# Kernel optimization log

Measured on AMD Instinct MI355X. Metric: run time of the kernel, lower is better.

The kernel has to match this reference:

```python
import jax, jax.numpy as jnp
import numpy as np

B, C, T = 16, 768, 9
S = T * T * T            # 729 tokens
H = 8                    # heads
E = 3                    # experts
HID = C * 4              # expert hidden dim (mult=4)


def setup_inputs() -> dict:
    key = jax.random.key(0)
    ks = jax.random.split(key, 8)
    w = lambda k, sh: (jax.random.normal(k, sh, jnp.float32) * 0.02)
    return {
        "x": jax.random.normal(ks[0], (B, C, T, T, T), jnp.float32),
        "ln_gamma": jnp.ones((C, T, T, T), jnp.float32),
        "ln_beta": jnp.zeros((C, T, T, T), jnp.float32),
        "w_qkv": w(ks[1], (C, 3 * C)),
        "w_out": w(ks[2], (C, C)),
        "w_gate": w(ks[3], (C, E)),
        "b_gate": jnp.zeros((E,), jnp.float32),
        "w1": w(ks[4], (E, C, HID)),
        "b1": jnp.zeros((E, HID), jnp.float32),
        "w2": w(ks[5], (E, HID, C)),
        "b2": jnp.zeros((E, C), jnp.float32),
    }


def reference(x, ln_gamma, ln_beta, w_qkv, w_out, w_gate, b_gate, w1, b1, w2, b2):
    b = x.shape[0]
    # LayerNorm over (C, T, H, W) per batch element, affine params [C,T,T,T]
    mu = jnp.mean(x, axis=(1, 2, 3, 4), keepdims=True)
    var = jnp.var(x, axis=(1, 2, 3, 4), keepdims=True)
    xn = (x - mu) * jax.lax.rsqrt(var + 1e-5) * ln_gamma + ln_beta

    # ---- attention (NOTE: source applies no 1/sqrt(d) scaling) ----
    tok = xn.reshape(b, C, S).transpose(0, 2, 1)                 # [b,s,c]
    qkv = (tok @ w_qkv).reshape(b, S, 3, H, C // H)              # [b,s,3,h,d]
    q = qkv[:, :, 0].transpose(0, 2, 1, 3)                       # [b,h,s,d]
    k = qkv[:, :, 1].transpose(0, 2, 1, 3)
    v = qkv[:, :, 2].transpose(0, 2, 1, 3)
    attn = jax.nn.softmax(jnp.einsum('bhqd,bhkd->bhqk', q, k), axis=-1)
    ctx = jnp.einsum('bhqk,bhkd->bqhd', attn, v).reshape(b, S, C)
    attn_out = (ctx @ w_out).transpose(0, 2, 1).reshape(b, C, T, T, T)
    x2 = x + attn_out                                            # residual (dropout = eval identity)

    # ---- switch-MoE (top-1 gate, all experts computed densely then masked) ----
    tok2 = x2.reshape(b, C, S).transpose(0, 2, 1)                # [b,s,c]
    gate = jax.nn.softmax(tok2 @ w_gate + b_gate, axis=-1)       # [b,s,E]
    mask = jax.nn.one_hot(jnp.argmax(gate, axis=-1), E, dtype=gate.dtype)
    mg = gate * mask
    denom = jnp.sum(mg, axis=0, keepdims=True) + 1e-6            # sum over dim 0, per source
    gate_scores = mg / denom * b                                 # capacity = int(1.0 * b)

    hmid = jax.nn.gelu(jnp.einsum('bsc,ech->bseh', tok2, w1) + b1, approximate=False)
    eout = jnp.einsum('bseh,ehc->bsec', hmid, w2) + b2           # [b,s,E,c]
    moe = jnp.einsum('bse,bsec->bsc', gate_scores, eout)         # weighted mix over experts

    out = x2 + moe.transpose(0, 2, 1).reshape(b, C, T, T, T)
    return out
```

## Files before the change

### kernel.cpp

```cpp
#include <hip/hip_runtime.h>

typedef __bf16 bf16;
typedef __bf16 bf16x4_t __attribute__((ext_vector_type(4)));
typedef __bf16 bf16x8_t __attribute__((ext_vector_type(8)));
typedef float f32x4 __attribute__((ext_vector_type(4)));

#define DEVI __device__ __forceinline__

#define N_B   16
#define N_C   768
#define N_S   729
#define N_TOK 11664
#define TOKP  11776
#define N_H   8
#define N_D   96
#define N_HID 3072
#define MOE_TILES 94
#define GATE_BLOCKS 183

#define OFF_WQKVH 0ull
#define OFF_WQKVL 3538944ull
#define OFF_WOUTH 7077888ull
#define OFF_WOUTL 8257536ull
#define OFF_W1T   9437184ull
#define OFF_W2T   23592960ull
#define OFF_XTOK  37748736ull
#define OFF_R3    73924608ull
#define OFF_TOKH  OFF_R3
#define OFF_TOKL  (OFF_R3 + 18087936ull)
#define OFF_VTH   OFF_R3
#define OFF_VTL   (OFF_R3 + 18087936ull)
#define OFF_T2H   OFF_R3
#define OFF_QKH   110100480ull
#define OFF_QKL   146276352ull
#define OFF_VPH   182452224ull
#define OFF_VPL   200540160ull
#define OFF_CTXH  OFF_VPH
#define OFF_CTXL  OFF_VPL
#define OFF_HMID  OFF_QKH
#define OFF_X2    218628096ull
#define OFF_STATS 254803968ull
#define OFF_DENOM (OFF_STATS + 256ull)
#define OFF_SEL   (OFF_STATS + 16384ull)
#define OFF_PVAL  (OFF_SEL + 65536ull)
#define OFF_GSV   (OFF_PVAL + 65536ull)
#define OFF_PERM  (OFF_GSV + 65536ull)
#define OFF_CNT   (OFF_PERM + 65536ull)

DEVI f32x4 mfma16(bf16x8_t a, bf16x8_t b, f32x4 c) {
  return __builtin_amdgcn_mfma_f32_16x16x32_bf16(a, b, c, 0, 0, 0);
}
DEVI bf16 f2bf(float f) { return (bf16)f; }
DEVI float bf2f(bf16 h) { return (float)h; }
#define GLDS(gp, lp) __builtin_amdgcn_global_load_lds( \
    (__attribute__((address_space(1))) void*)(gp),     \
    (__attribute__((address_space(3))) void*)(lp), 16, 0, 0)

template<bool SPLIT>
__global__ void kxpose(const float* __restrict__ in, bf16* __restrict__ oh,
                       bf16* __restrict__ ol, int R, int Cc) {
  __shared__ float T[32][33];
  int c0 = blockIdx.x * 32, r0 = blockIdx.y * 32;
  int tx = threadIdx.x, ty = threadIdx.y;
#pragma unroll
  for (int i = 0; i < 4; i++)
    T[ty + i * 8][tx] = in[(size_t)(r0 + ty + i * 8) * Cc + c0 + tx];
  __syncthreads();
#pragma unroll
  for (int i = 0; i < 4; i++) {
    float v = T[tx][ty + i * 8];
    size_t o = (size_t)(c0 + ty + i * 8) * R + r0 + tx;
    bf16 hh = f2bf(v);
    oh[o] = hh;
    if constexpr (SPLIT) ol[o] = f2bf(v - bf2f(hh));
  }
}

__global__ __launch_bounds__(256) void ln_stats(const float* __restrict__ x,
                                                double* __restrict__ stats) {
  int b = blockIdx.x >> 7, ch = blockIdx.x & 127;
  const float* xb = x + (size_t)b * 559872;
  int start = ch * 4374;
  float s = 0.f, ss = 0.f;
  for (int i = start + threadIdx.x; i < start + 4374; i += 256) {
    float v = xb[i];
    s += v; ss += v * v;
  }
#pragma unroll
  for (int o = 32; o > 0; o >>= 1) { s += __shfl_down(s, o); ss += __shfl_down(ss, o); }
  __shared__ float rs[4], rss[4];
  int w = threadIdx.x >> 6;
  if ((threadIdx.x & 63) == 0) { rs[w] = s; rss[w] = ss; }
  __syncthreads();
  if (threadIdx.x == 0) {
    atomicAdd(&stats[b * 2 + 0], (double)(rs[0] + rs[1] + rs[2] + rs[3]));
    atomicAdd(&stats[b * 2 + 1], (double)(rss[0] + rss[1] + rss[2] + rss[3]));
  }
}

__global__ void ln_apply(const float* __restrict__ x, const float* __restrict__ g,
                         const float* __restrict__ be, const double* __restrict__ stats,
                         float* __restrict__ xtok, bf16* __restrict__ th, bf16* __restrict__ tl) {
  __shared__ float TN[32][33], TX[32][33];
  int b = blockIdx.z, c0 = blockIdx.y * 32, s0 = blockIdx.x * 32;
  double mu = stats[b * 2] * (1.0 / 559872.0);
  double var = stats[b * 2 + 1] * (1.0 / 559872.0) - mu * mu;
  float rstd = (float)(1.0 / sqrt(var + 1e-5));
  float muf = (float)mu;
  int tx = threadIdx.x, ty = threadIdx.y;
  size_t bo = (size_t)b * 559872;
#pragma unroll
  for (int i = 0; i < 4; i++) {
    int c = c0 + ty + i * 8, s = s0 + tx;
    float v = 0.f, xn = 0.f;
    if (s < N_S) {
      v = x[bo + (size_t)c * 729 + s];
      xn = (v - muf) * rstd * g[(size_t)c * 729 + s] + be[(size_t)c * 729 + s];
    }
    TX[ty + i * 8][tx] = v;
    TN[ty + i * 8][tx] = xn;
  }
  __syncthreads();
#pragma unroll
  for (int i = 0; i < 4; i++) {
    int s = s0 + ty + i * 8;
    if (s < N_S) {
      size_t tok = (size_t)b * 729 + s;
      int c = c0 + tx;
      float xv = TX[tx][ty + i * 8];
      float xn = TN[tx][ty + i * 8];
      xtok[tok * 768 + c] = xv;
      bf16 hh = f2bf(xn);
      th[tok * 768 + c] = hh;
      tl[tok * 768 + c] = f2bf(xn - bf2f(hh));
    }
  }
}

enum { EPI_HL = 0, EPI_ATTNOUT = 1 };

template<int EPI, bool SPLIT>
__global__ __launch_bounds__(256, 2)
void gemm_k(const bf16* __restrict__ Ah, const bf16* __restrict__ Al,
            const bf16* __restrict__ Bh, const bf16* __restrict__ Bl,
            int M, int N, int K,
            bf16* __restrict__ o0, bf16* __restrict__ o1, float* __restrict__ of,
            const float* __restrict__ fa) {
  __shared__ bf16 Ash[4096], Bsh[4096], Asl[4096], Bsl[4096];
  const int t = threadIdx.x;
  const int lane = t & 63, w = t >> 6;
  const int wr = (w >> 1) << 6, wc = (w & 1) << 6;
  const int lr = lane & 15, lg = lane >> 4;
  const size_t arow = (size_t)blockIdx.y * 128;
  const size_t brow = (size_t)blockIdx.x * 128;
  const int sr = t >> 2, sc4 = (t & 3) << 3;
  const bf16* pA0 = Ah + (arow + sr) * (size_t)K + sc4;
  const bf16* pA1 = pA0 + ((size_t)K << 6);
  const bf16* pB0 = Bh + (brow + sr) * (size_t)K + sc4;
  const bf16* pB1 = pB0 + ((size_t)K << 6);
  const bf16 *pA0l = nullptr, *pA1l = nullptr, *pB0l = nullptr, *pB1l = nullptr;
  if constexpr (SPLIT) {
    pA0l = Al + (arow + sr) * (size_t)K + sc4; pA1l = pA0l + ((size_t)K << 6);
    pB0l = Bl + (brow + sr) * (size_t)K + sc4; pB1l = pB0l + ((size_t)K << 6);
  }
  f32x4 acc[4][4] = {};
  for (int k0 = 0; k0 < K; k0 += 32) {
    __syncthreads();
    GLDS(pA0 + k0, &Ash[t * 8]);
    GLDS(pA1 + k0, &Ash[2048 + t * 8]);
    GLDS(pB0 + k0, &Bsh[t * 8]);
    GLDS(pB1 + k0, &Bsh[2048 + t * 8]);
    if constexpr (SPLIT) {
      GLDS(pA0l + k0, &Asl[t * 8]);
      GLDS(pA1l + k0, &Asl[2048 + t * 8]);
      GLDS(pB0l + k0, &Bsl[t * 8]);
      GLDS(pB1l + k0, &Bsl[2048 + t * 8]);
    }
    asm volatile("s_waitcnt vmcnt(0)" ::: "memory");
    __syncthreads();
    bf16x8_t af[4], bq[4], afl[4], bql[4];
#pragma unroll
    for (int m = 0; m < 4; m++) {
      int row = wr + m * 16 + lr;
      af[m] = *(const bf16x8_t*)&Ash[row * 32 + lg * 8];
      if constexpr (SPLIT) afl[m] = *(const bf16x8_t*)&Asl[row * 32 + lg * 8];
    }
#pragma unroll
    for (int n = 0; n < 4; n++) {
      int row = wc + n * 16 + lr;
      bq[n] = *(const bf16x8_t*)&Bsh[row * 32 + lg * 8];
      if constexpr (SPLIT) bql[n] = *(const bf16x8_t*)&Bsl[row * 32 + lg * 8];
    }
#pragma unroll
    for (int m = 0; m < 4; m++)
#pragma unroll
      for (int n = 0; n < 4; n++) {
        acc[m][n] = mfma16(af[m], bq[n], acc[m][n]);
        if constexpr (SPLIT) {
          acc[m][n] = mfma16(af[m], bql[n], acc[m][n]);
          acc[m][n] = mfma16(afl[m], bq[n], acc[m][n]);
        }
      }
  }
#pragma unroll
  for (int m = 0; m < 4; m++) {
#pragma unroll
    for (int r = 0; r < 4; r++) {
      int gr = (int)arow + wr + m * 16 + lg * 4 + r;
      if (gr >= M) continue;
#pragma unroll
      for (int n = 0; n < 4; n++) {
        int gc = (int)brow + wc + n * 16 + lr;
        float v = acc[m][n][r];
        size_t oidx = (size_t)gr * N + gc;
        if constexpr (EPI == EPI_HL) {
          bf16 hh = f2bf(v);
          o0[oidx] = hh;
          o1[oidx] = f2bf(v - bf2f(hh));
        } else {
          float x2v = v + fa[(size_t)gr * 768 + gc];
          of[(size_t)gr * 768 + gc] = x2v;
          o0[(size_t)gr * 768 + gc] = f2bf(x2v);
        }
      }
    }
  }
}

__global__ __launch_bounds__(256, 2)
void gemm_moe1(const bf16* __restrict__ Ah, const bf16* __restrict__ W1T,
               const float* __restrict__ b1, const int* __restrict__ perm,
               const int* __restrict__ poff, bf16* __restrict__ hmid) {
  const int arow = blockIdx.y * 128;
  if (arow >= poff[3]) return;
  const int e = (arow >= poff[1]) + (arow >= poff[2]);
  const bf16* Bh = W1T + (size_t)e * 3072 * 768;
  const float* bias = b1 + e * 3072;
  __shared__ bf16 Ash[4096], Bsh[4096];
  const int t = threadIdx.x;
  const int lane = t & 63, w = t >> 6;
  const int wr = (w >> 1) << 6, wc = (w & 1) << 6;
  const int lr = lane & 15, lg = lane >> 4;
  const size_t brow = (size_t)blockIdx.x * 128;
  const int sr = t >> 2, sc4 = (t & 3) << 3;
  int i0 = perm[arow + sr];       if (i0 < 0) i0 = 0;
  int i1 = perm[arow + sr + 64];  if (i1 < 0) i1 = 0;
  const bf16* pA0 = Ah + (size_t)i0 * 768 + sc4;
  const bf16* pA1 = Ah + (size_t)i1 * 768 + sc4;
  const bf16* pB0 = Bh + (brow + sr) * 768 + sc4;
  const bf16* pB1 = pB0 + (768ull << 6);
  f32x4 acc[4][4] = {};
  for (int k0 = 0; k0 < 768; k0 += 32) {
    __syncthreads();
    GLDS(pA0 + k0, &Ash[t * 8]);
    GLDS(pA1 + k0, &Ash[2048 + t * 8]);
    GLDS(pB0 + k0, &Bsh[t * 8]);
    GLDS(pB1 + k0, &Bsh[2048 + t * 8]);
    asm volatile("s_waitcnt vmcnt(0)" ::: "memory");
    __syncthreads();
    bf16x8_t af[4], bq[4];
#pragma unroll
    for (int m = 0; m < 4; m++)
      af[m] = *(const bf16x8_t*)&Ash[(wr + m * 16 + lr) * 32 + lg * 8];
#pragma unroll
    for (int n = 0; n < 4; n++)
      bq[n] = *(const bf16x8_t*)&Bsh[(wc + n * 16 + lr) * 32 + lg * 8];
#pragma unroll
    for (int m = 0; m < 4; m++)
#pragma unroll
      for (int n = 0; n < 4; n++)
        acc[m][n] = mfma16(af[m], bq[n], acc[m][n]);
  }
#pragma unroll
  for (int m = 0; m < 4; m++)
#pragma unroll
    for (int r = 0; r < 4; r++) {
      int gr = arow + wr + m * 16 + lg * 4 + r;
#pragma unroll
      for (int n = 0; n < 4; n++) {
        int gc = (int)brow + wc + n * 16 + lr;
        float z = acc[m][n][r] + bias[gc];
        float gl = 0.5f * z * (1.f + erff(z * 0.7071067811865476f));
        hmid[(size_t)gr * 3072 + gc] = f2bf(gl);
      }
    }
}

__global__ __launch_bounds__(256, 2)
void gemm_moe2(const bf16* __restrict__ hmid, const bf16* __restrict__ W2T,
               const float* __restrict__ b2, const int* __restrict__ perm,
               const int* __restrict__ poff, const float* __restrict__ gsv,
               float* __restrict__ moe) {
  const int arow = blockIdx.y * 128;
  if (arow >= poff[3]) return;
  const int e = (arow >= poff[1]) + (arow >= poff[2]);
  const bf16* Bh = W2T + (size_t)e * 768 * 3072;
  const float* bias = b2 + e * 768;
  __shared__ bf16 Ash[4096], Bsh[4096];
  const int t = threadIdx.x;
  const int lane = t & 63, w = t >> 6;
  const int wr = (w >> 1) << 6, wc = (w & 1) << 6;
  const int lr = lane & 15, lg = lane >> 4;
  const size_t brow = (size_t)blockIdx.x * 128;
  const int sr = t >> 2, sc4 = (t & 3) << 3;
  const bf16* pA0 = hmid + (size_t)(arow + sr) * 3072 + sc4;
  const bf16* pA1 = pA0 + (3072ull << 6);
  const bf16* pB0 = Bh + (brow + sr) * 3072 + sc4;
  const bf16* pB1 = pB0 + (3072ull << 6);
  f32x4 acc[4][4] = {};
  for (int k0 = 0; k0 < 3072; k0 += 32) {
    __syncthreads();
    GLDS(pA0 + k0, &Ash[t * 8]);
    GLDS(pA1 + k0, &Ash[2048 + t * 8]);
    GLDS(pB0 + k0, &Bsh[t * 8]);
    GLDS(pB1 + k0, &Bsh[2048 + t * 8]);
    asm volatile("s_waitcnt vmcnt(0)" ::: "memory");
    __syncthreads();
    bf16x8_t af[4], bq[4];
#pragma unroll
    for (int m = 0; m < 4; m++)
      af[m] = *(const bf16x8_t*)&Ash[(wr + m * 16 + lr) * 32 + lg * 8];
#pragma unroll
    for (int n = 0; n < 4; n++)
      bq[n] = *(const bf16x8_t*)&Bsh[(wc + n * 16 + lr) * 32 + lg * 8];
#pragma unroll
    for (int m = 0; m < 4; m++)
#pragma unroll
      for (int n = 0; n < 4; n++)
        acc[m][n] = mfma16(af[m], bq[n], acc[m][n]);
  }
#pragma unroll
  for (int m = 0; m < 4; m++)
#pragma unroll
    for (int r = 0; r < 4; r++) {
      int gr = arow + wr + m * 16 + lg * 4 + r;
      int tok = perm[gr];
      if (tok < 0) continue;
      float gv = gsv[tok];
#pragma unroll
      for (int n = 0; n < 4; n++) {
        int gc = (int)brow + wc + n * 16 + lr;
        moe[(size_t)tok * 768 + gc] = (acc[m][n][r] + bias[gc]) * gv;
      }
    }
}

__global__ __launch_bounds__(256) void repack_v(const bf16* __restrict__ vph,
    const bf16* __restrict__ vpl, bf16* __restrict__ vth, bf16* __restrict__ vtl) {
  __shared__ bf16 Lh[96][40], Ll[96][40];
  int t = threadIdx.x;
  int bh = blockIdx.y, b = bh >> 3, h = bh & 7;
  int s0 = blockIdx.x * 32;
  for (int v = t; v < 384; v += 256) {
    int e0 = v * 8;
    int r = e0 / 96;
    int c = e0 - r * 96;
    size_t src = ((size_t)b * 729 + s0 + r) * 768 + h * 96 + c;
    bf16x8_t xh = *(const bf16x8_t*)&vph[src];
    bf16x8_t xl = *(const bf16x8_t*)&vpl[src];
    bool ok = (s0 + r) < N_S;
#pragma unroll
    for (int j = 0; j < 8; j++) {
      Lh[c + j][r] = ok ? xh[j] : f2bf(0.f);
      Ll[c + j][r] = ok ? xl[j] : f2bf(0.f);
    }
  }
  __syncthreads();
  for (int vv = t; vv < 768; vv += 256) {
    int e0 = vv * 4;
    int d = e0 >> 5, sl = e0 & 31;
    bf16x4_t ohv, olv;
#pragma unroll
    for (int j = 0; j < 4; j++) { ohv[j] = Lh[d][sl + j]; olv[j] = Ll[d][sl + j]; }
    size_t dst = (size_t)bh * (96ull * 736ull) + (size_t)d * 736 + s0 + sl;
    *(bf16x4_t*)&vth[dst] = ohv;
    *(bf16x4_t*)&vtl[dst] = olv;
  }
}

DEVI int pslot(int w, int s) { return ((s >> 9) << 11) + (w << 9) + (s & 511); }

__global__ __launch_bounds__(256, 3)
void attn(const bf16* __restrict__ qkh, const bf16* __restrict__ qkl,
          const bf16* __restrict__ vth, const bf16* __restrict__ vtl,
          bf16* __restrict__ ch, bf16* __restrict__ cl) {
  __shared__ bf16 Ksh[6144], Ksl[6144], Vsh[6144], Vsl[6144];
  const int t = threadIdx.x, lane = t & 63, w = t >> 6;
  const int lr = lane & 15, lg = lane >> 4;
  const int bh = blockIdx.y, b = bh >> 3, h = bh & 7;
  const int q0 = blockIdx.x * 64;
  const size_t tokbase = (size_t)b * 729;
  const int qr = w * 16 + lr;
  const size_t qrow = (tokbase + q0 + qr) * 1536ull + (size_t)h * 96;
  bf16x8_t qh[3], ql[3];
#pragma unroll
  for (int ks = 0; ks < 3; ks++) {
    qh[ks] = *(const bf16x8_t*)&qkh[qrow + ks * 32 + lg * 8];
    ql[ks] = *(const bf16x8_t*)&qkl[qrow + ks * 32 + lg * 8];
  }

  auto loadK = [&](int kt) {
    const int kv0 = kt * 64;
#pragma unroll
    for (int chk = 0; chk < 3; chk++) {
      int kv = t >> 2, dg = t & 3;
      int sdg = dg ^ (kv & 3);
      size_t ksrc = (tokbase + kv0 + kv) * 1536ull + 768ull + (size_t)h * 96 + chk * 32 + (sdg << 3);
      int ldsoff = chk * 2048 + t * 8;
      GLDS(qkh + ksrc, &Ksh[ldsoff]);
      GLDS(qkl + ksrc, &Ksl[ldsoff]);
    }
  };
  auto loadV = [&](int kt) {
    const int kv0 = kt * 64;
#pragma unroll
    for (int chk = 0; chk < 3; chk++) {
      int ldsoff = chk * 2048 + t * 8;
      int d = ldsoff >> 6;
      int grp = (ldsoff >> 3) & 7;
      int sg = grp ^ (d & 7);
      size_t vsrc = (size_t)bh * (96ull * 736ull) + (size_t)d * 736 + kv0 + (sg << 3);
      GLDS(vth + vsrc, &Vsh[ldsoff]);
      GLDS(vtl + vsrc, &Vsl[ldsoff]);
    }
  };

  float mrow[4] = {-1e30f, -1e30f, -1e30f, -1e30f};
  float lpart[4] = {0.f, 0.f, 0.f, 0.f};
  f32x4 octx[6] = {};

  loadK(0);
  asm volatile("s_waitcnt vmcnt(0)" ::: "memory");
  __syncthreads();
  loadV(0);

  for (int kt = 0; kt < 12; kt++) {
    const int kv0 = kt * 64;
    f32x4 sc[4];
    __builtin_amdgcn_s_setprio(1);
#pragma unroll
    for (int cf = 0; cf < 4; cf++) {
      f32x4 a = {0.f, 0.f, 0.f, 0.f};
      int kvrow = cf * 16 + lr;
#pragma unroll
      for (int ks = 0; ks < 3; ks++) {
        int slot = ks * 2048 + kvrow * 32 + ((lg ^ (kvrow & 3)) << 3);
        bf16x8_t kh = *(const bf16x8_t*)&Ksh[slot];
        bf16x8_t kl = *(const bf16x8_t*)&Ksl[slot];
        a = mfma16(qh[ks], kh, a);
        a = mfma16(qh[ks], kl, a);
        a = mfma16(ql[ks], kh, a);
      }
      if (kv0 + kvrow >= N_S) { a[0] = -1e30f; a[1] = -1e30f; a[2] = -1e30f; a[3] = -1e30f; }
      sc[cf] = a;
    }
    __builtin_amdgcn_s_setprio(0);
    float lmax[4];
#pragma unroll
    for (int r = 0; r < 4; r++)
      lmax[r] = fmaxf(fmaxf(sc[0][r], sc[1][r]), fmaxf(sc[2][r], sc[3][r]));
    bool ok = (lmax[0] <= mrow[0] + 8.f) && (lmax[1] <= mrow[1] + 8.f) &&
              (lmax[2] <= mrow[2] + 8.f) && (lmax[3] <= mrow[3] + 8.f);
    if (!__all(ok)) {
      float escv[4];
#pragma unroll
      for (int r = 0; r < 4; r++) {
        float a = lmax[r];
#pragma unroll
        for (int o = 1; o < 16; o <<= 1) a = fmaxf(a, __shfl_xor(a, o));
        float mn = fmaxf(mrow[r], a);
        escv[r] = __expf(mrow[r] - mn);
        mrow[r] = mn;
        lpart[r] *= escv[r];
      }
#pragma unroll
      for (int df = 0; df < 6; df++)
#pragma unroll
        for (int r = 0; r < 4; r++) octx[df][r] *= escv[r];
    }
#pragma unroll
    for (int cf = 0; cf < 4; cf++)
#pragma unroll
      for (int r = 0; r < 4; r++) {
        float p = __expf(sc[cf][r] - mrow[r]);
        sc[cf][r] = p;
        lpart[r] += p;
      }
    asm volatile("s_waitcnt vmcnt(0)" ::: "memory");
    __syncthreads();
#pragma unroll
    for (int cf = 0; cf < 4; cf++)
#pragma unroll
      for (int r = 0; r < 4; r++) {
        int qloc = lg * 4 + r;
        int kvg = (cf << 1) | (lr >> 3);
        int xw = (qloc ^ (qloc >> 2)) & 7;
        int slot = qloc * 64 + (((kvg ^ xw) << 3) | (lr & 7));
        float p = sc[cf][r];
        bf16 hp = f2bf(p);
        int ps = pslot(w, slot);
        Ksh[ps] = hp;
        Ksl[ps] = f2bf(p - bf2f(hp));
      }
    asm volatile("s_waitcnt lgkmcnt(0)" ::: "memory");
    __builtin_amdgcn_sched_barrier(0);
    bf16x8_t pah[2], pal[2];
#pragma unroll
    for (int ks = 0; ks < 2; ks++) {
      int xr = (lr ^ (lr >> 2)) & 7;
      int slot = lr * 64 + ((((ks << 2) | lg) ^ xr) << 3);
      int ps = pslot(w, slot);
      pah[ks] = *(const bf16x8_t*)&Ksh[ps];
      pal[ks] = *(const bf16x8_t*)&Ksl[ps];
    }
    asm volatile("s_waitcnt lgkmcnt(0)" ::: "memory");
    __builtin_amdgcn_sched_barrier(0);
    if (kt < 11) loadK(kt + 1);
    __builtin_amdgcn_s_setprio(1);
#pragma unroll
    for (int df = 0; df < 6; df++) {
      int dd = df * 16 + lr;
#pragma unroll
      for (int ks = 0; ks < 2; ks++) {
        int slot = dd * 64 + ((((ks << 2) | lg) ^ (dd & 7)) << 3);
        bf16x8_t vh = *(const bf16x8_t*)&Vsh[slot];
        bf16x8_t vl = *(const bf16x8_t*)&Vsl[slot];
        octx[df] = mfma16(pah[ks], vh, octx[df]);
        octx[df] = mfma16(pah[ks], vl, octx[df]);
        octx[df] = mfma16(pal[ks], vh, octx[df]);
      }
    }
    __builtin_amdgcn_s_setprio(0);
    if (kt < 11) {
      asm volatile("s_waitcnt vmcnt(0)" ::: "memory");
      __syncthreads();
      loadV(kt + 1);
    }
  }
  float lrow[4];
#pragma unroll
  for (int r = 0; r < 4; r++) {
    float a = lpart[r];
#pragma unroll
    for (int o = 1; o < 16; o <<= 1) a += __shfl_xor(a, o);
    lrow[r] = a;
  }
#pragma unroll
  for (int r = 0; r < 4; r++) {
    int qloc = w * 16 + lg * 4 + r;
    if (q0 + qloc >= N_S) continue;
    size_t orow = (tokbase + q0 + qloc) * 768ull + (size_t)h * 96;
    float inv = 1.f / lrow[r];
#pragma unroll
    for (int df = 0; df < 6; df++) {
      float v = octx[df][r] * inv;
      bf16 hh = f2bf(v);
      ch[orow + df * 16 + lr] = hh;
      cl[orow + df * 16 + lr] = f2bf(v - bf2f(hh));
    }
  }
}

__global__ __launch_bounds__(256) void gate_k(const float* __restrict__ x2,
    const float* __restrict__ wg, const float* __restrict__ bg,
    int* __restrict__ sel, float* __restrict__ pval, float* __restrict__ denom,
    int* __restrict__ cnt) {
  int lane = threadIdx.x & 63, w = threadIdx.x >> 6;
  float wv[12][3];
#pragma unroll
  for (int j = 0; j < 12; j++) {
    int c = lane + j * 64;
    const float* wgc = wg + c * 3;
    wv[j][0] = wgc[0]; wv[j][1] = wgc[1]; wv[j][2] = wgc[2];
  }
  float bg0 = bg[0], bg1 = bg[1], bg2 = bg[2];
  int cloc0 = 0, cloc1 = 0, cloc2 = 0;
  int base_tok = (blockIdx.x * 4 + w) * 16;
  for (int it = 0; it < 16; it++) {
    int tok = base_tok + it;
    if (tok >= N_TOK) break;
    const float* row = x2 + (size_t)tok * 768;
    double a0 = 0, a1 = 0, a2 = 0;
#pragma unroll
    for (int j = 0; j < 12; j++) {
      float xv = row[lane + j * 64];
      a0 += (double)(xv * wv[j][0]);
      a1 += (double)(xv * wv[j][1]);
      a2 += (double)(xv * wv[j][2]);
    }
#pragma unroll
    for (int o = 32; o > 0; o >>= 1) {
      a0 += __shfl_down(a0, o);
      a1 += __shfl_down(a1, o);
      a2 += __shfl_down(a2, o);
    }
    if (lane == 0) {
      float g0 = (float)a0 + bg0, g1 = (float)a1 + bg1, g2 = (float)a2 + bg2;
      float mx = fmaxf(g0, fmaxf(g1, g2));
      float e0 = __expf(g0 - mx), e1 = __expf(g1 - mx), e2 = __expf(g2 - mx);
      float inv = 1.f / (e0 + e1 + e2);
      int am = 0; float pm = e0;
      if (e1 > pm) { pm = e1; am = 1; }
      if (e2 > pm) { pm = e2; am = 2; }
      float p = pm * inv;
      sel[tok] = am;
      pval[tok] = p;
      int s = tok - (tok / 729) * 729;
      atomicAdd(&denom[s * 3 + am], p);
      cloc0 += (am == 0); cloc1 += (am == 1); cloc2 += (am == 2);
    }
  }
  __shared__ int bc[3];
  if (threadIdx.x == 0) { bc[0] = 0; bc[1] = 0; bc[2] = 0; }
  __syncthreads();
  if (lane == 0) {
    if (cloc0) atomicAdd(&bc[0], cloc0);
    if (cloc1) atomicAdd(&bc[1], cloc1);
    if (cloc2) atomicAdd(&bc[2], cloc2);
  }
  __syncthreads();
  if (threadIdx.x < 3 && bc[threadIdx.x]) atomicAdd(&cnt[threadIdx.x], bc[threadIdx.x]);
}

__global__ void moe_scan(const int* __restrict__ cnt, int* __restrict__ poff) {
  int p1 = (cnt[0] + 127) & ~127;
  int p2 = p1 + ((cnt[1] + 127) & ~127);
  int p3 = p2 + ((cnt[2] + 127) & ~127);
  poff[0] = 0; poff[1] = p1; poff[2] = p2; poff[3] = p3;
}

__global__ __launch_bounds__(256) void moe_scatter(const int* __restrict__ sel,
                            const float* __restrict__ pval,
                            const float* __restrict__ denom, const int* __restrict__ poff,
                            int* __restrict__ cur, int* __restrict__ perm,
                            float* __restrict__ gsv) {
  int tok = blockIdx.x * 256 + threadIdx.x;
  int lane = threadIdx.x & 63, w = threadIdx.x >> 6;
  bool valid = tok < N_TOK;
  int e = valid ? sel[tok] : -1;
  if (valid) {
    int s = tok - (tok / 729) * 729;
    gsv[tok] = pval[tok] * 16.f / (denom[s * 3 + e] + 1e-6f);
  }
  unsigned long long m0 = __ballot(e == 0);
  unsigned long long m1 = __ballot(e == 1);
  unsigned long long m2 = __ballot(e == 2);
  __shared__ int wcnt[4][3], wbase[4][3];
  if (lane == 0) {
    wcnt[w][0] = __popcll(m0);
    wcnt[w][1] = __popcll(m1);
    wcnt[w][2] = __popcll(m2);
  }
  __syncthreads();
  if (threadIdx.x < 3) {
    int x = threadIdx.x;
    int c0 = wcnt[0][x], c1 = wcnt[1][x], c2 = wcnt[2][x], c3 = wcnt[3][x];
    int base = atomicAdd(&cur[x], c0 + c1 + c2 + c3);
    wbase[0][x] = base;
    wbase[1][x] = base + c0;
    wbase[2][x] = base + c0 + c1;
    wbase[3][x] = base + c0 + c1 + c2;
  }
  __syncthreads();
  if (valid) {
    unsigned long long lt = (lane == 0) ? 0ull : ((~0ull) >> (64 - lane));
    unsigned long long me = (e == 0) ? m0 : (e == 1) ? m1 : m2;
    int pos = wbase[w][e] + __popcll(me & lt);
    perm[poff[e] + pos] = tok;
  }
}

__global__ void final_k(const float* __restrict__ x2, const float* __restrict__ moe,
                        float* __restrict__ out) {
  __shared__ float L[32][33];
  int b = blockIdx.z, c0 = blockIdx.y * 32, s0 = blockIdx.x * 32;
  int tx = threadIdx.x, ty = threadIdx.y;
#pragma unroll
  for (int i = 0; i < 4; i++) {
    int s = s0 + ty + i * 8;
    float v = 0.f;
    if (s < N_S) {
      size_t tok = (size_t)b * 729 + s;
      v = x2[tok * 768 + c0 + tx] + moe[tok * 768 + c0 + tx];
    }
    L[ty + i * 8][tx] = v;
  }
  __syncthreads();
#pragma unroll
  for (int i = 0; i < 4; i++) {
    int s = s0 + tx;
    int c = c0 + ty + i * 8;
    if (s < N_S) out[((size_t)b * 768 + c) * 729 + s] = L[tx][ty + i * 8];
  }
}

extern "C" void kernel_launch(void* const* d_in, const int* in_sizes, int n_in,
                              void* d_out, int out_size, void* d_ws, size_t ws_size,
                              hipStream_t stream) {
  (void)in_sizes; (void)n_in; (void)out_size; (void)ws_size;
  const float* x     = (const float*)d_in[0];
  const float* lng   = (const float*)d_in[1];
  const float* lnb   = (const float*)d_in[2];
  const float* wqkv  = (const float*)d_in[3];
  const float* wout  = (const float*)d_in[4];
  const float* wgate = (const float*)d_in[5];
  const float* bgate = (const float*)d_in[6];
  const float* w1    = (const float*)d_in[7];
  const float* b1    = (const float*)d_in[8];
  const float* w2    = (const float*)d_in[9];
  const float* b2    = (const float*)d_in[10];
  float* out = (float*)d_out;
  char* ws = (char*)d_ws;

  bf16* WQKVH = (bf16*)(ws + OFF_WQKVH);
  bf16* WQKVL = (bf16*)(ws + OFF_WQKVL);
  bf16* WOUTH = (bf16*)(ws + OFF_WOUTH);
  bf16* WOUTL = (bf16*)(ws + OFF_WOUTL);
  bf16* W1T   = (bf16*)(ws + OFF_W1T);
  bf16* W2T   = (bf16*)(ws + OFF_W2T);
  float* XTOK = (float*)(ws + OFF_XTOK);
  float* MOE  = (float*)(ws + OFF_XTOK);
  bf16* TOKH  = (bf16*)(ws + OFF_TOKH);
  bf16* TOKL  = (bf16*)(ws + OFF_TOKL);
  bf16* VTH   = (bf16*)(ws + OFF_VTH);
  bf16* VTL   = (bf16*)(ws + OFF_VTL);
  bf16* T2H   = (bf16*)(ws + OFF_T2H);
  bf16* QKH   = (bf16*)(ws + OFF_QKH);
  bf16* QKL   = (bf16*)(ws + OFF_QKL);
  bf16* VPH   = (bf16*)(ws + OFF_VPH);
  bf16* VPL   = (bf16*)(ws + OFF_VPL);
  bf16* CTXH  = (bf16*)(ws + OFF_CTXH);
  bf16* CTXL  = (bf16*)(ws + OFF_CTXL);
  bf16* HMID  = (bf16*)(ws + OFF_HMID);
  float* X2   = (float*)(ws + OFF_X2);
  double* STATS = (double*)(ws + OFF_STATS);
  float* DENOM  = (float*)(ws + OFF_DENOM);
  int*   SEL    = (int*)(ws + OFF_SEL);
  float* PVAL   = (float*)(ws + OFF_PVAL);
  float* GSV    = (float*)(ws + OFF_GSV);
  int*   PERM   = (int*)(ws + OFF_PERM);
  int*   CNT    = (int*)(ws + OFF_CNT);
  int*   POFF   = CNT + 4;
  int*   CUR    = CNT + 8;

  hipMemsetAsync(ws + OFF_STATS, 0, 16384, stream);
  hipMemsetAsync(ws + OFF_CNT, 0, 64, stream);
  hipMemsetAsync(ws + OFF_PERM, 0xFF, MOE_TILES * 128 * 4, stream);

  dim3 tb(32, 8);
  kxpose<true><<<dim3(72, 24), tb, 0, stream>>>(wqkv, WQKVH, WQKVL, 768, 2304);
  kxpose<true><<<dim3(24, 24), tb, 0, stream>>>(wout, WOUTH, WOUTL, 768, 768);
  for (int e = 0; e < 3; e++) {
    kxpose<false><<<dim3(96, 24), tb, 0, stream>>>(w1 + (size_t)e * 768 * 3072,
        W1T + (size_t)e * 3072 * 768, nullptr, 768, 3072);
    kxpose<false><<<dim3(24, 96), tb, 0, stream>>>(w2 + (size_t)e * 3072 * 768,
        W2T + (size_t)e * 768 * 3072, nullptr, 3072, 768);
  }
  ln_stats<<<2048, 256, 0, stream>>>(x, STATS);
  ln_apply<<<dim3(23, 24, 16), tb, 0, stream>>>(x, lng, lnb, STATS, XTOK, TOKH, TOKL);
  gemm_k<EPI_HL, true><<<dim3(12, 92), 256, 0, stream>>>(
      TOKH, TOKL, WQKVH, WQKVL, N_TOK, 1536, 768, QKH, QKL, nullptr, nullptr);
  gemm_k<EPI_HL, true><<<dim3(6, 92), 256, 0, stream>>>(
      TOKH, TOKL, WQKVH + 1536 * 768, WQKVL + 1536 * 768, N_TOK, 768, 768,
      VPH, VPL, nullptr, nullptr);
  repack_v<<<dim3(23, 128), 256, 0, stream>>>(VPH, VPL, VTH, VTL);
  attn<<<dim3(12, 128), 256, 0, stream>>>(QKH, QKL, VTH, VTL, CTXH, CTXL);
  gemm_k<EPI_ATTNOUT, true><<<dim3(6, 92), 256, 0, stream>>>(
      CTXH, CTXL, WOUTH, WOUTL, N_TOK, 768, 768, T2H, nullptr, X2, XTOK);
  gate_k<<<GATE_BLOCKS, 256, 0, stream>>>(X2, wgate, bgate, SEL, PVAL, DENOM, CNT);
  moe_scan<<<1, 1, 0, stream>>>(CNT, POFF);
  moe_scatter<<<46, 256, 0, stream>>>(SEL, PVAL, DENOM, POFF, CUR, PERM, GSV);
  gemm_moe1<<<dim3(24, MOE_TILES), 256, 0, stream>>>(T2H, W1T, b1, PERM, POFF, HMID);
  gemm_moe2<<<dim3(6, MOE_TILES), 256, 0, stream>>>(HMID, W2T, b2, PERM, POFF, GSV, MOE);
  final_k<<<dim3(23, 24, 16), tb, 0, stream>>>(X2, MOE, out);
}
```

Measured before the change: 732.7 us.

## Double GEMM K-tile to 64 with XOR-swizzled LDS layout

All three GEMM kernels (generic split-bf16 GEMM and both MoE expert GEMMs) now stage 64-wide K slices instead of 32, halving the number of barrier/wait iterations per tile. The LDS layout is XOR-swizzled by row so the wider 128-byte rows avoid bank conflicts on the fragment reads. MoE kernels also raise the occupancy hint to 3 blocks per CU. The change doubles LDS per block (64KB for the split GEMM), which may limit occupancy and conflict with the raised launch bound.

New measurement: 707.8 us. 1.04x faster.

```diff
diff --git a/kernel.cpp b/kernel.cpp
--- a/kernel.cpp
+++ b/kernel.cpp
@@ -146,61 +146,66 @@
             int M, int N, int K,
             bf16* __restrict__ o0, bf16* __restrict__ o1, float* __restrict__ of,
             const float* __restrict__ fa) {
-  __shared__ bf16 Ash[4096], Bsh[4096], Asl[4096], Bsl[4096];
+  __shared__ __align__(16) bf16 Ash[8192], Bsh[8192];
+  __shared__ __align__(16) bf16 Asl[SPLIT ? 8192 : 8], Bsl[SPLIT ? 8192 : 8];
   const int t = threadIdx.x;
   const int lane = t & 63, w = t >> 6;
   const int wr = (w >> 1) << 6, wc = (w & 1) << 6;
   const int lr = lane & 15, lg = lane >> 4;
   const size_t arow = (size_t)blockIdx.y * 128;
   const size_t brow = (size_t)blockIdx.x * 128;
-  const int sr = t >> 2, sc4 = (t & 3) << 3;
-  const bf16* pA0 = Ah + (arow + sr) * (size_t)K + sc4;
-  const bf16* pA1 = pA0 + ((size_t)K << 6);
-  const bf16* pB0 = Bh + (brow + sr) * (size_t)K + sc4;
-  const bf16* pB1 = pB0 + ((size_t)K << 6);
-  const bf16 *pA0l = nullptr, *pA1l = nullptr, *pB0l = nullptr, *pB1l = nullptr;
+  const int sr = t >> 3;
+  const int sg = ((t & 7) ^ (sr & 7)) << 3;
+  const bf16* pA = Ah + (arow + sr) * (size_t)K + sg;
+  const bf16* pB = Bh + (brow + sr) * (size_t)K + sg;
+  const bf16 *pAl = nullptr, *pBl = nullptr;
   if constexpr (SPLIT) {
-    pA0l = Al + (arow + sr) * (size_t)K + sc4; pA1l = pA0l + ((size_t)K << 6);
-    pB0l = Bl + (brow + sr) * (size_t)K + sc4; pB1l = pB0l + ((size_t)K << 6);
-  }
+    pAl = Al + (arow + sr) * (size_t)K + sg;
+    pBl = Bl + (brow + sr) * (size_t)K + sg;
+  }
+  const size_t rstep = (size_t)K << 5;
   f32x4 acc[4][4] = {};
-  for (int k0 = 0; k0 < K; k0 += 32) {
+  for (int k0 = 0; k0 < K; k0 += 64) {
     __syncthreads();
-    GLDS(pA0 + k0, &Ash[t * 8]);
-    GLDS(pA1 + k0, &Ash[2048 + t * 8]);
-    GLDS(pB0 + k0, &Bsh[t * 8]);
-    GLDS(pB1 + k0, &Bsh[2048 + t * 8]);
-    if constexpr (SPLIT) {
-      GLDS(pA0l + k0, &Asl[t * 8]);
-      GLDS(pA1l + k0, &Asl[2048 + t * 8]);
-      GLDS(pB0l + k0, &Bsl[t * 8]);
-      GLDS(pB1l + k0, &Bsl[2048 + t * 8]);
+#pragma unroll
+    for (int c = 0; c < 4; c++) {
+      GLDS(pA + c * rstep + k0, &Ash[c * 2048 + t * 8]);
+      GLDS(pB + c * rstep + k0, &Bsh[c * 2048 + t * 8]);
+      if constexpr (SPLIT) {
+        GLDS(pAl + c * rstep + k0, &Asl[c * 2048 + t * 8]);
+        GLDS(pBl + c * rstep + k0, &Bsl[c * 2048 + t * 8]);
+      }
     }
     asm volatile("s_waitcnt vmcnt(0)" ::: "memory");
     __syncthreads();
-    bf16x8_t af[4], bq[4], afl[4], bql[4];
-#pragma unroll
-    for (int m = 0; m < 4; m++) {
-      int row = wr + m * 16 + lr;
-      af[m] = *(const bf16x8_t*)&Ash[row * 32 + lg * 8];
-      if constexpr (SPLIT) afl[m] = *(const bf16x8_t*)&Asl[row * 32 + lg * 8];
-    }
-#pragma unroll
-    for (int n = 0; n < 4; n++) {
-      int row = wc + n * 16 + lr;
-      bq[n] = *(const bf16x8_t*)&Bsh[row * 32 + lg * 8];
-      if constexpr (SPLIT) bql[n] = *(const bf16x8_t*)&Bsl[row * 32 + lg * 8];
-    }
-#pragma unroll
-    for (int m = 0; m < 4; m++)
+#pragma unroll
+    for (int kk = 0; kk < 2; kk++) {
+      bf16x8_t af[4], bq[4], afl[4], bql[4];
+#pragma unroll
+      for (int m = 0; m < 4; m++) {
+        int row = wr + m * 16 + lr;
+        int off = row * 64 + ((((kk << 2) | lg) ^ (row & 7)) << 3);
+        af[m] = *(const bf16x8_t*)&Ash[off];
+        if constexpr (SPLIT) afl[m] = *(const bf16x8_t*)&Asl[off];
+      }
 #pragma unroll
       for (int n = 0; n < 4; n++) {
-        acc[m][n] = mfma16(af[m], bq[n], acc[m][n]);
-        if constexpr (SPLIT) {
-          acc[m][n] = mfma16(af[m], bql[n], acc[m][n]);
-          acc[m][n] = mfma16(afl[m], bq[n], acc[m][n]);
+        int row = wc + n * 16 + lr;
+        int off = row * 64 + ((((kk << 2) | lg) ^ (row & 7)) << 3);
+        bq[n] = *(const bf16x8_t*)&Bsh[off];
+        if constexpr (SPLIT) bql[n] = *(const bf16x8_t*)&Bsl[off];
+      }
+#pragma unroll
+      for (int m = 0; m < 4; m++)
+#pragma unroll
+        for (int n = 0; n < 4; n++) {
+          acc[m][n] = mfma16(af[m], bq[n], acc[m][n]);
+          if constexpr (SPLIT) {
+            acc[m][n] = mfma16(af[m], bql[n], acc[m][n]);
+            acc[m][n] = mfma16(afl[m], bq[n], acc[m][n]);
+          }
         }
-      }
+    }
   }
 #pragma unroll
   for (int m = 0; m < 4; m++) {
@@ -227,7 +232,7 @@
   }
 }
 
-__global__ __launch_bounds__(256, 2)
+__global__ __launch_bounds__(256, 3)
 void gemm_moe1(const bf16* __restrict__ Ah, const bf16* __restrict__ W1T,
                const float* __restrict__ b1, const int* __restrict__ perm,
                const int* __restrict__ poff, bf16* __restrict__ hmid) {
@@ -236,40 +241,51 @@
   const int e = (arow >= poff[1]) + (arow >= poff[2]);
   const bf16* Bh = W1T + (size_t)e * 3072 * 768;
   const float* bias = b1 + e * 3072;
-  __shared__ bf16 Ash[4096], Bsh[4096];
+  __shared__ __align__(16) bf16 Ash[8192], Bsh[8192];
   const int t = threadIdx.x;
   const int lane = t & 63, w = t >> 6;
   const int wr = (w >> 1) << 6, wc = (w & 1) << 6;
   const int lr = lane & 15, lg = lane >> 4;
   const size_t brow = (size_t)blockIdx.x * 128;
-  const int sr = t >> 2, sc4 = (t & 3) << 3;
-  int i0 = perm[arow + sr];       if (i0 < 0) i0 = 0;
-  int i1 = perm[arow + sr + 64];  if (i1 < 0) i1 = 0;
-  const bf16* pA0 = Ah + (size_t)i0 * 768 + sc4;
-  const bf16* pA1 = Ah + (size_t)i1 * 768 + sc4;
-  const bf16* pB0 = Bh + (brow + sr) * 768 + sc4;
-  const bf16* pB1 = pB0 + (768ull << 6);
+  const int sr = t >> 3;
+  const int sg = ((t & 7) ^ (sr & 7)) << 3;
+  int ip[4];
+#pragma unroll
+  for (int c = 0; c < 4; c++) {
+    int ii = perm[arow + c * 32 + sr];
+    ip[c] = (ii < 0) ? 0 : ii;
+  }
+  const bf16* pB = Bh + (brow + sr) * 768 + sg;
+  const size_t rstep = 768ull << 5;
   f32x4 acc[4][4] = {};
-  for (int k0 = 0; k0 < 768; k0 += 32) {
+  for (int k0 = 0; k0 < 768; k0 += 64) {
     __syncthreads();
-    GLDS(pA0 + k0, &Ash[t * 8]);
-    GLDS(pA1 + k0, &Ash[2048 + t * 8]);
-    GLDS(pB0 + k0, &Bsh[t * 8]);
-    GLDS(pB1 + k0, &Bsh[2048 + t * 8]);
+#pragma unroll
+    for (int c = 0; c < 4; c++) {
+      GLDS(Ah + (size_t)ip[c] * 768 + sg + k0, &Ash[c * 2048 + t * 8]);
+      GLDS(pB + c * rstep + k0, &Bsh[c * 2048 + t * 8]);
+    }
     asm volatile("s_waitcnt vmcnt(0)" ::: "memory");
     __syncthreads();
-    bf16x8_t af[4], bq[4];
-#pragma unroll
-    for (int m = 0; m < 4; m++)
-      af[m] = *(const bf16x8_t*)&Ash[(wr + m * 16 + lr) * 32 + lg * 8];
-#pragma unroll
-    for (int n = 0; n < 4; n++)
-      bq[n] = *(const bf16x8_t*)&Bsh[(wc + n * 16 + lr) * 32 + lg * 8];
-#pragma unroll
-    for (int m = 0; m < 4; m++)
-#pragma unroll
-      for (int n = 0; n < 4; n++)
-        acc[m][n] = mfma16(af[m], bq[n], acc[m][n]);
+#pragma unroll
+    for (int kk = 0; kk < 2; kk++) {
+      bf16x8_t af[4], bq[4];
+#pragma unroll
+      for (int m = 0; m < 4; m++) {
+        int row = wr + m * 16 + lr;
+        af[m] = *(const bf16x8_t*)&Ash[row * 64 + ((((kk << 2) | lg) ^ (row & 7)) << 3)];
+      }
+#pragma unroll
+      for (int n = 0; n < 4; n++) {
+        int row = wc + n * 16 + lr;
+        bq[n] = *(const bf16x8_t*)&Bsh[row * 64 + ((((kk << 2) | lg) ^ (row & 7)) << 3)];
+      }
+#pragma unroll
+      for (int m = 0; m < 4; m++)
+#pragma unroll
+        for (int n = 0; n < 4; n++)
+          acc[m][n] = mfma16(af[m], bq[n], acc[m][n]);
+    }
   }
 #pragma unroll
   for (int m = 0; m < 4; m++)
@@ -286,7 +302,7 @@
     }
 }
 
-__global__ __launch_bounds__(256, 2)
+__global__ __launch_bounds__(256, 3)
 void gemm_moe2(const bf16* __restrict__ hmid, const bf16* __restrict__ W2T,
                const float* __restrict__ b2, const int* __restrict__ perm,
                const int* __restrict__ poff, const float* __restrict__ gsv,
@@ -296,38 +312,46 @@
   const int e = (arow >= poff[1]) + (arow >= poff[2]);
   const bf16* Bh = W2T + (size_t)e * 768 * 3072;
   const float* bias = b2 + e * 768;
-  __shared__ bf16 Ash[4096], Bsh[4096];
+  __shared__ __align__(16) bf16 Ash[8192], Bsh[8192];
   const int t = threadIdx.x;
   const int lane = t & 63, w = t >> 6;
   const int wr = (w >> 1) << 6, wc = (w & 1) << 6;
   const int lr = lane & 15, lg = lane >> 4;
   const size_t brow = (size_t)blockIdx.x * 128;
-  const int sr = t >> 2, sc4 = (t & 3) << 3;
-  const bf16* pA0 = hmid + (size_t)(arow + sr) * 3072 + sc4;
-  const bf16* pA1 = pA0 + (3072ull << 6);
-  const bf16* pB0 = Bh + (brow + sr) * 3072 + sc4;
-  const bf16* pB1 = pB0 + (3072ull << 6);
+  const int sr = t >> 3;
+  const int sg = ((t & 7) ^ (sr & 7)) << 3;
+  const bf16* pA = hmid + (size_t)(arow + sr) * 3072 + sg;
+  const bf16* pB = Bh + (brow + sr) * 3072 + sg;
+  const size_t rstep = 3072ull << 5;
   f32x4 acc[4][4] = {};
-  for (int k0 = 0; k0 < 3072; k0 += 32) {
+  for (int k0 = 0; k0 < 3072; k0 += 64) {
     __syncthreads();
-    GLDS(pA0 + k0, &Ash[t * 8]);
-    GLDS(pA1 + k0, &Ash[2048 + t * 8]);
-    GLDS(pB0 + k0, &Bsh[t * 8]);
-    GLDS(pB1 + k0, &Bsh[2048 + t * 8]);
+#pragma unroll
+    for (int c = 0; c < 4; c++) {
+      GLDS(pA + c * rstep + k0, &Ash[c * 2048 + t * 8]);
+      GLDS(pB + c * rstep + k0, &Bsh[c * 2048 + t * 8]);
+    }
     asm volatile("s_waitcnt vmcnt(0)" ::: "memory");
     __syncthreads();
-    bf16x8_t af[4], bq[4];
-#pragma unroll
-    for (int m = 0; m < 4; m++)
-      af[m] = *(const bf16x8_t*)&Ash[(wr + m * 16 + lr) * 32 + lg * 8];
-#pragma unroll
-    for (int n = 0; n < 4; n++)
-      bq[n] = *(const bf16x8_t*)&Bsh[(wc + n * 16 + lr) * 32 + lg * 8];
-#pragma unroll
-    for (int m = 0; m < 4; m++)
-#pragma unroll
-      for (int n = 0; n < 4; n++)
-        acc[m][n] = mfma16(af[m], bq[n], acc[m][n]);
+#pragma unroll
+    for (int kk = 0; kk < 2; kk++) {
+      bf16x8_t af[4], bq[4];
+#pragma unroll
+      for (int m = 0; m < 4; m++) {
+        int row = wr + m * 16 + lr;
+        af[m] = *(const bf16x8_t*)&Ash[row * 64 + ((((kk << 2) | lg) ^ (row & 7)) << 3)];
+      }
+#pragma unroll
+      for (int n = 0; n < 4; n++) {
+        int row = wc + n * 16 + lr;
+        bq[n] = *(const bf16x8_t*)&Bsh[row * 64 + ((((kk << 2) | lg) ^ (row & 7)) << 3)];
+      }
+#pragma unroll
+      for (int m = 0; m < 4; m++)
+#pragma unroll
+        for (int n = 0; n < 4; n++)
+          acc[m][n] = mfma16(af[m], bq[n], acc[m][n]);
+    }
   }
 #pragma unroll
   for (int m = 0; m < 4; m++)
```
